# Performance work log

Measured on AMD Instinct MI355X. Metric: run time of the kernel, lower is better.

Reference implementation:

```python
import jax, jax.numpy as jnp
import numpy as np

QUALITY = 50

# standard JPEG luminance / chrominance quantization tables
_Y_TABLE = np.array([
    [16, 11, 10, 16, 24, 40, 51, 61],
    [12, 12, 14, 19, 26, 58, 60, 55],
    [14, 13, 16, 24, 40, 57, 69, 56],
    [14, 17, 22, 29, 51, 87, 80, 62],
    [18, 22, 37, 56, 68, 109, 103, 77],
    [24, 35, 55, 64, 81, 104, 113, 92],
    [49, 64, 78, 87, 103, 121, 120, 101],
    [72, 92, 95, 98, 112, 100, 103, 99]], dtype=np.float32)
_C_TABLE = np.full((8, 8), 99., dtype=np.float32)
_C_TABLE[:4, :4] = np.array([[17, 18, 24, 47], [18, 21, 26, 66],
                             [24, 26, 56, 99], [47, 66, 99, 99]], dtype=np.float32)

_i = np.arange(8)
_A = np.cos((2 * _i[:, None] + 1) * _i[None, :] * np.pi / 16).astype(np.float32)
_alpha = np.array([1.0 / np.sqrt(2)] + [1.0] * 7, dtype=np.float32)
_ALPHA2 = np.outer(_alpha, _alpha).astype(np.float32)        # idct pre-scale
_SCALE = (_ALPHA2 * 0.25).astype(np.float32)                 # dct post-scale

_RGB2YCC = np.array([[0.299, 0.587, 0.114],
                     [-0.168736, -0.331264, 0.5],
                     [0.5, -0.418688, -0.081312]], dtype=np.float32)
_SHIFT1 = np.array([0., 128., 128.], dtype=np.float32)
_YCC2RGB = np.array([[1., 0., 1.402],
                     [1., -0.344136, -0.714136],
                     [1., 1.772, 0.]], dtype=np.float32)
_SHIFT2 = np.array([0., -128., -128.], dtype=np.float32)


def _diff_round(x):
    r = jnp.round(x)
    return r + (x - r) ** 3


def _jpeg_channel(ch, table, factor):
    # ch: [B, h, w] -> blockwise DCT / quantize / dequant / IDCT -> [B, h, w]
    b, h, w = ch.shape
    blocks = ch.reshape(b, h // 8, 8, w // 8, 8).transpose(0, 1, 3, 2, 4).reshape(b, -1, 8, 8)
    A = jnp.asarray(_A)
    dct = jnp.asarray(_SCALE) * jnp.einsum('bnxy,xu,yv->bnuv', blocks - 128., A, A)
    qt = jnp.asarray(table) * factor
    q = _diff_round(dct / qt)
    deq = q * qt
    idct = 0.25 * jnp.einsum('bnuv,ux,vy->bnxy', deq * jnp.asarray(_ALPHA2), A, A) + 128.
    return idct.reshape(b, h // 8, w // 8, 8, 8).transpose(0, 1, 3, 2, 4).reshape(b, h, w)


def _diff_jpeg(x, quality):
    # quality -> scaling factor
    q = float(quality)
    factor = (5000. / q if q < 50 else 200. - 2. * q) / 100.
    x = jnp.clip(x, 0., 1.)
    img = jnp.transpose(x, (0, 2, 3, 1)) * 255.                      # [B,H,W,3]
    ycc = img @ jnp.asarray(_RGB2YCC).T + jnp.asarray(_SHIFT1)
    y, cb, cr = ycc[..., 0], ycc[..., 1], ycc[..., 2]
    b, h, w = y.shape
    # 4:2:0 chroma subsampling via 2x2 average pooling
    cb_s = cb.reshape(b, h // 2, 2, w // 2, 2).mean(axis=(2, 4))
    cr_s = cr.reshape(b, h // 2, 2, w // 2, 2).mean(axis=(2, 4))
    y2 = _jpeg_channel(y, _Y_TABLE, factor)
    cb2 = _jpeg_channel(cb_s, _C_TABLE, factor)
    cr2 = _jpeg_channel(cr_s, _C_TABLE, factor)
    cb_u = jnp.repeat(jnp.repeat(cb2, 2, axis=1), 2, axis=2)
    cr_u = jnp.repeat(jnp.repeat(cr2, 2, axis=1), 2, axis=2)
    ycc2 = jnp.stack([y2, cb_u, cr_u], axis=-1)
    rgb = (ycc2 + jnp.asarray(_SHIFT2)) @ jnp.asarray(_YCC2RGB).T
    rgb = jnp.clip(rgb, 0., 255.) / 255.
    out = jnp.transpose(rgb, (0, 3, 1, 2))                           # back to NCHW
    return jnp.clip(out, 0., 1.)


def setup_inputs() -> dict:
    key = jax.random.key(0)
    x = jax.random.uniform(key, (32, 3, 512, 512), dtype=jnp.float32)
    return {"x": x}


def reference(x):
    return _diff_jpeg(x, QUALITY)
```

## Files before the change

### kernel.cpp

```cpp
#include <hip/hip_runtime.h>
#include <math.h>

#define HH 512
#define WW 512

typedef float f2 __attribute__((ext_vector_type(2)));
typedef float f4 __attribute__((ext_vector_type(4)));

#define YS2  36
#define CS2  18
#define OY   0
#define OCB  576
#define OCR  720
#define OSCR 864
#define OAB  OSCR
#define WSZ  1272

static __device__ __forceinline__ f4 vclamp01x255(f4 v) {
    f4 z = 0.f, one = 1.f;
    return __builtin_elementwise_max(__builtin_elementwise_min(v, one), z) * 255.f;
}

__device__ __constant__ float YTAB[64] = {
    16,11,10,16,24,40,51,61,
    12,12,14,19,26,58,60,55,
    14,13,16,24,40,57,69,56,
    14,17,22,29,51,87,80,62,
    18,22,37,56,68,109,103,77,
    24,35,55,64,81,104,113,92,
    49,64,78,87,103,121,120,101,
    72,92,95,98,112,100,103,99};
__device__ __constant__ float CTAB[64] = {
    17,18,24,47,99,99,99,99,
    18,21,26,66,99,99,99,99,
    24,26,56,99,99,99,99,99,
    47,66,99,99,99,99,99,99,
    99,99,99,99,99,99,99,99,
    99,99,99,99,99,99,99,99,
    99,99,99,99,99,99,99,99,
    99,99,99,99,99,99,99,99};

__global__ __launch_bounds__(256) void jpeg_fused(const float* __restrict__ in,
                                                  float* __restrict__ out)
{
#pragma clang fp contract(off)
    __shared__ float Wall[4][WSZ];

    const int tid  = threadIdx.x;
    const int wid  = tid >> 6;
    const int lane = tid & 63;
    float* W = Wall[wid];

    const int wv    = blockIdx.x * 4 + wid;
    const int b     = wv >> 8;
    const int strip = (wv >> 3) & 31;
    const int seg   = wv & 7;
    const int h0    = strip * 16;
    const int w0    = seg * 64;
    const size_t plane = (size_t)HH * WW;

    const int rp  = lane >> 3;
    const int pr  = rp * 2;
    const int c4  = (lane & 7) * 4;
    const size_t grow   = ((size_t)b * 3 * HH + (size_t)(h0 + pr)) * WW + c4;
    const size_t gbase0 = grow + w0;
    const size_t gbase1 = grow + w0 + 32;

    const int g = lane >> 3, j = lane & 7;
    f2 As2[32];

    auto loadT = [&](f4* L, size_t gb) {
        L[0] = *(const f4*)(in + gb);
        L[1] = *(const f4*)(in + gb + WW);
        L[2] = *(const f4*)(in + gb + plane);
        L[3] = *(const f4*)(in + gb + plane + WW);
        L[4] = *(const f4*)(in + gb + 2 * plane);
        L[5] = *(const f4*)(in + gb + 2 * plane + WW);
    };

    auto stageT = [&](const f4* L) {
#pragma clang fp contract(off)
        f4 r0 = vclamp01x255(L[0]), r1 = vclamp01x255(L[1]);
        f4 g0 = vclamp01x255(L[2]), g1 = vclamp01x255(L[3]);
        f4 b0 = vclamp01x255(L[4]), b1 = vclamp01x255(L[5]);
        f4 y0  = ((r0 * 0.299f)     + (g0 * 0.587f))     + (b0 * 0.114f);
        f4 y1  = ((r1 * 0.299f)     + (g1 * 0.587f))     + (b1 * 0.114f);
        f4 cb0 = ((r0 * -0.168736f) + (g0 * -0.331264f)) + (b0 * 0.5f);
        f4 cb1 = ((r1 * -0.168736f) + (g1 * -0.331264f)) + (b1 * 0.5f);
        f4 cr0 = ((r0 * 0.5f)       + (g0 * -0.418688f)) + (b0 * -0.081312f);
        f4 cr1 = ((r1 * 0.5f)       + (g1 * -0.418688f)) + (b1 * -0.081312f);
        cb0 = cb0 + 128.f; cb1 = cb1 + 128.f;
        cr0 = cr0 + 128.f; cr1 = cr1 + 128.f;
        y0 = y0 - 128.f;  y1 = y1 - 128.f;
        *(f4*)&W[OY + pr * YS2 + c4]       = y0;
        *(f4*)&W[OY + (pr + 1) * YS2 + c4] = y1;
        f2 mb, mr;
        {
            float s01 = cb0.x + cb0.y, s23 = cb1.x + cb1.y;
            mb[0] = (s01 + s23) / 4.0f;
            float t01 = cb0.z + cb0.w, t23 = cb1.z + cb1.w;
            mb[1] = (t01 + t23) / 4.0f;
        }
        {
            float s01 = cr0.x + cr0.y, s23 = cr1.x + cr1.y;
            mr[0] = (s01 + s23) / 4.0f;
            float t01 = cr0.z + cr0.w, t23 = cr1.z + cr1.w;
            mr[1] = (t01 + t23) / 4.0f;
        }
        *(f2*)&W[OCB + rp * CS2 + (lane & 7) * 2] = mb;
        *(f2*)&W[OCR + rp * CS2 + (lane & 7) * 2] = mr;
    };

    auto dctAll = [&]() {
#pragma clang fp contract(off)
#pragma unroll
        for (int pass = 0; pass < 2; ++pass) {
            if (g < 6) {
                const int it   = pass * 6 + g;
                const bool isY = (it < 8);
                float* scr = &W[OSCR + g * 68];

                float X[8];
                int by = 0, bx = 0, ob = 0;
                if (isY) {
                    by = it >> 2; bx = it & 3;
#pragma unroll
                    for (int x = 0; x < 8; ++x)
                        X[x] = W[OY + (by * 8 + x) * YS2 + bx * 8 + j];
                } else {
                    ob = (it < 10) ? OCB : OCR;
                    bx = (it < 10) ? (it - 8) : (it - 10);
#pragma unroll
                    for (int x = 0; x < 8; ++x)
                        X[x] = W[ob + x * CS2 + bx * 8 + j] - 128.f;
                }

                f2 Tv[4];
#pragma unroll
                for (int m = 0; m < 4; ++m) {
                    f2 a = {0.f, 0.f};
#pragma unroll
                    for (int x = 0; x < 8; ++x) {
                        f2 xx = {X[x], X[x]};
                        a = __builtin_elementwise_fma(xx, As2[x * 4 + m], a);
                    }
                    Tv[m] = a;
                }
#pragma unroll
                for (int m = 0; m < 4; ++m) {
                    scr[(2 * m) * 8 + j]     = Tv[m][0];
                    scr[(2 * m + 1) * 8 + j] = Tv[m][1];
                }
                float Tt[8];
                {
                    float4 a = *(const float4*)&scr[j * 8];
                    float4 c = *(const float4*)&scr[j * 8 + 4];
                    Tt[0] = a.x; Tt[1] = a.y; Tt[2] = a.z; Tt[3] = a.w;
                    Tt[4] = c.x; Tt[5] = c.y; Tt[6] = c.z; Tt[7] = c.w;
                }
                float R[8];
#pragma unroll
                for (int m = 0; m < 4; ++m) {
                    f2 a = {0.f, 0.f};
#pragma unroll
                    for (int y = 0; y < 8; ++y) {
                        f2 tt = {Tt[y], Tt[y]};
                        a = __builtin_elementwise_fma(tt, As2[y * 4 + m], a);
                    }
                    R[2 * m] = a[0]; R[2 * m + 1] = a[1];
                }
                const float* QT = isY ? YTAB : CTAB;
                float qt[8];
                {
                    float4 a = *(const float4*)&QT[j * 8];
                    float4 c = *(const float4*)&QT[j * 8 + 4];
                    qt[0] = a.x; qt[1] = a.y; qt[2] = a.z; qt[3] = a.w;
                    qt[4] = c.x; qt[5] = c.y; qt[6] = c.z; qt[7] = c.w;
                }
                const float RC = 0.70710678118654752440f;
                float au = (j == 0) ? RC : 1.0f;
                float G[8];
#pragma unroll
                for (int v = 0; v < 8; ++v) {
                    float av    = (v == 0) ? RC : 1.0f;
                    float a2    = au * av;
                    float scale = a2 * 0.25f;
                    float dct   = scale * R[v];
                    float xq    = dct / qt[v];
                    float rd    = rintf(xq);
                    float d     = xq - rd;
                    float cube  = (d * d) * d;
                    float qq    = rd + cube;
                    float deq   = qq * qt[v];
                    G[v] = deq * a2;
                }
#pragma unroll
                for (int v = 0; v < 8; ++v) scr[v * 8 + j] = G[v];
                float Gt[8];
                {
                    float4 a = *(const float4*)&scr[j * 8];
                    float4 c = *(const float4*)&scr[j * 8 + 4];
                    Gt[0] = a.x; Gt[1] = a.y; Gt[2] = a.z; Gt[3] = a.w;
                    Gt[4] = c.x; Gt[5] = c.y; Gt[6] = c.z; Gt[7] = c.w;
                }
                f2 T2v[4];
#pragma unroll
                for (int m = 0; m < 4; ++m) {
                    f2 a = {0.f, 0.f};
#pragma unroll
                    for (int u = 0; u < 8; ++u) {
                        f2 gg = {Gt[u], Gt[u]};
                        a = __builtin_elementwise_fma(gg, As2[u * 4 + m], a);
                    }
                    T2v[m] = a;
                }
#pragma unroll
                for (int m = 0; m < 4; ++m) {
                    scr[(2 * m) * 8 + j]     = T2v[m][0];
                    scr[(2 * m + 1) * 8 + j] = T2v[m][1];
                }
                float T2t[8];
                {
                    float4 a = *(const float4*)&scr[j * 8];
                    float4 c = *(const float4*)&scr[j * 8 + 4];
                    T2t[0] = a.x; T2t[1] = a.y; T2t[2] = a.z; T2t[3] = a.w;
                    T2t[4] = c.x; T2t[5] = c.y; T2t[6] = c.z; T2t[7] = c.w;
                }
                float O[8];
#pragma unroll
                for (int m = 0; m < 4; ++m) {
                    f2 a = {0.f, 0.f};
#pragma unroll
                    for (int v = 0; v < 8; ++v) {
                        f2 tt = {T2t[v], T2t[v]};
                        a = __builtin_elementwise_fma(tt, As2[v * 4 + m], a);
                    }
                    a = (a * 0.25f) + 128.f;
                    O[2 * m] = a[0]; O[2 * m + 1] = a[1];
                }
                if (isY) {
                    *(f4*)&W[OY + (by * 8 + j) * YS2 + bx * 8]     = (f4){O[0], O[1], O[2], O[3]};
                    *(f4*)&W[OY + (by * 8 + j) * YS2 + bx * 8 + 4] = (f4){O[4], O[5], O[6], O[7]};
                } else {
                    *(f4*)&W[ob + j * CS2 + bx * 8]     = (f4){O[0], O[1], O[2], O[3]};
                    *(f4*)&W[ob + j * CS2 + bx * 8 + 4] = (f4){O[4], O[5], O[6], O[7]};
                }
            }
            asm volatile("" ::: "memory");
        }
    };

    auto outputT = [&](size_t gb) {
#pragma clang fp contract(off)
        const float INV255 = 1.0f / 255.0f;
        f4 ya = *(const f4*)&W[OY + pr * YS2 + c4];
        f4 yb = *(const f4*)&W[OY + (pr + 1) * YS2 + c4];
        f2 cbp = *(const f2*)&W[OCB + rp * CS2 + (lane & 7) * 2];
        f2 crp = *(const f2*)&W[OCR + rp * CS2 + (lane & 7) * 2];
        float cb0 = cbp[0] - 128.f, cb1 = cbp[1] - 128.f;
        float cr0 = crp[0] - 128.f, cr1 = crp[1] - 128.f;
        f4 cbm = {cb0, cb0, cb1, cb1};
        f4 crm = {cr0, cr0, cr1, cr1};
        f4 z = 0.f, m255 = 255.f;
#pragma unroll
        for (int row = 0; row < 2; ++row) {
            f4 yy = row ? yb : ya;
            f4 rv = yy + (crm * 1.402f);
            f4 gv = (yy + (cbm * -0.344136f)) + (crm * -0.714136f);
            f4 bv = yy + (cbm * 1.772f);
            rv = __builtin_elementwise_max(__builtin_elementwise_min(rv, m255), z) * INV255;
            gv = __builtin_elementwise_max(__builtin_elementwise_min(gv, m255), z) * INV255;
            bv = __builtin_elementwise_max(__builtin_elementwise_min(bv, m255), z) * INV255;
            size_t base = gb + (size_t)row * WW;
            __builtin_nontemporal_store(rv, (f4*)(out + base));
            __builtin_nontemporal_store(gv, (f4*)(out + base + plane));
            __builtin_nontemporal_store(bv, (f4*)(out + base + 2 * plane));
        }
    };

    f4 L1[6], L2[6];
    loadT(L1, gbase0);

    {
        int x = lane >> 3, u = lane & 7;
        double arg = (double)((2 * x + 1) * u) * 3.14159265358979323846 / 16.0;
        W[OAB + lane] = (float)cos(arg);
    }
#pragma unroll
    for (int k = 0; k < 32; ++k) {
        As2[k][0] = __int_as_float(__builtin_amdgcn_readfirstlane(__float_as_int(W[OAB + 2 * k])));
        As2[k][1] = __int_as_float(__builtin_amdgcn_readfirstlane(__float_as_int(W[OAB + 2 * k + 1])));
    }
    asm volatile("" ::: "memory");

    stageT(L1);
    loadT(L2, gbase1);
    asm volatile("" ::: "memory");
    dctAll();
    outputT(gbase0);
    asm volatile("" ::: "memory");
    stageT(L2);
    asm volatile("" ::: "memory");
    dctAll();
    outputT(gbase1);
}

extern "C" void kernel_launch(void* const* d_in, const int* in_sizes, int n_in,
                              void* d_out, int out_size, void* d_ws, size_t ws_size,
                              hipStream_t stream)
{
    const float* x = (const float*)d_in[0];
    float* o = (float*)d_out;
    int batch  = in_sizes[0] / (3 * HH * WW);
    int blocks = batch * 256 / 4;
    jpeg_fused<<<blocks, 256, 0, stream>>>(x, o);
}
```

Measured before the change: 41.00 us.

## Stage full 16x64 tile, run DCT in place across all lanes, use reciprocal quantization

Each wave now stages both 32-column halves into shared memory at once, with wider row strides, and issues both global loads up front. The blockwise DCT/IDCT then runs in three passes where all 8 lane-groups are busy: two Y passes and one chroma pass. Before, there were two passes of 6 active groups per half, four in all. The transposes reuse the block's own shared-memory region instead of a separate scratch area. Quantization division is replaced by a reciprocal multiply plus one Newton-style FMA correction, meant to match IEEE division, which cuts divide cost but raises shared-memory use per block (which may lower occupancy) and keeps more registers live for both loads.

```diff
diff --git a/kernel.cpp b/kernel.cpp
--- a/kernel.cpp
+++ b/kernel.cpp
@@ -7,14 +7,14 @@
 typedef float f2 __attribute__((ext_vector_type(2)));
 typedef float f4 __attribute__((ext_vector_type(4)));
 
-#define YS2  36
-#define CS2  18
+#define WFENCE() asm volatile("" ::: "memory")
+
+#define YS3  68
+#define CS3  36
 #define OY   0
-#define OCB  576
-#define OCR  720
-#define OSCR 864
-#define OAB  OSCR
-#define WSZ  1272
+#define OCB  1088
+#define OCR  1376
+#define WSZ  1664
 
 static __device__ __forceinline__ f4 vclamp01x255(f4 v) {
     f4 z = 0.f, one = 1.f;
@@ -39,6 +39,24 @@
     99,99,99,99,99,99,99,99,
     99,99,99,99,99,99,99,99,
     99,99,99,99,99,99,99,99};
+__device__ __constant__ float YINV[64] = {
+    1.f/16,1.f/11,1.f/10,1.f/16,1.f/24,1.f/40,1.f/51,1.f/61,
+    1.f/12,1.f/12,1.f/14,1.f/19,1.f/26,1.f/58,1.f/60,1.f/55,
+    1.f/14,1.f/13,1.f/16,1.f/24,1.f/40,1.f/57,1.f/69,1.f/56,
+    1.f/14,1.f/17,1.f/22,1.f/29,1.f/51,1.f/87,1.f/80,1.f/62,
+    1.f/18,1.f/22,1.f/37,1.f/56,1.f/68,1.f/109,1.f/103,1.f/77,
+    1.f/24,1.f/35,1.f/55,1.f/64,1.f/81,1.f/104,1.f/113,1.f/92,
+    1.f/49,1.f/64,1.f/78,1.f/87,1.f/103,1.f/121,1.f/120,1.f/101,
+    1.f/72,1.f/92,1.f/95,1.f/98,1.f/112,1.f/100,1.f/103,1.f/99};
+__device__ __constant__ float CINV[64] = {
+    1.f/17,1.f/18,1.f/24,1.f/47,1.f/99,1.f/99,1.f/99,1.f/99,
+    1.f/18,1.f/21,1.f/26,1.f/66,1.f/99,1.f/99,1.f/99,1.f/99,
+    1.f/24,1.f/26,1.f/56,1.f/99,1.f/99,1.f/99,1.f/99,1.f/99,
+    1.f/47,1.f/66,1.f/99,1.f/99,1.f/99,1.f/99,1.f/99,1.f/99,
+    1.f/99,1.f/99,1.f/99,1.f/99,1.f/99,1.f/99,1.f/99,1.f/99,
+    1.f/99,1.f/99,1.f/99,1.f/99,1.f/99,1.f/99,1.f/99,1.f/99,
+    1.f/99,1.f/99,1.f/99,1.f/99,1.f/99,1.f/99,1.f/99,1.f/99,
+    1.f/99,1.f/99,1.f/99,1.f/99,1.f/99,1.f/99,1.f/99,1.f/99};
 
 __global__ __launch_bounds__(256) void jpeg_fused(const float* __restrict__ in,
                                                   float* __restrict__ out)
@@ -61,7 +79,8 @@
 
     const int rp  = lane >> 3;
     const int pr  = rp * 2;
-    const int c4  = (lane & 7) * 4;
+    const int c8  = lane & 7;
+    const int c4  = c8 * 4;
     const size_t grow   = ((size_t)b * 3 * HH + (size_t)(h0 + pr)) * WW + c4;
     const size_t gbase0 = grow + w0;
     const size_t gbase1 = grow + w0 + 32;
@@ -78,7 +97,7 @@
         L[5] = *(const f4*)(in + gb + 2 * plane + WW);
     };
 
-    auto stageT = [&](const f4* L) {
+    auto stageT = [&](const f4* L, int P) {
 #pragma clang fp contract(off)
         f4 r0 = vclamp01x255(L[0]), r1 = vclamp01x255(L[1]);
         f4 g0 = vclamp01x255(L[2]), g1 = vclamp01x255(L[3]);
@@ -92,8 +111,8 @@
         cb0 = cb0 + 128.f; cb1 = cb1 + 128.f;
         cr0 = cr0 + 128.f; cr1 = cr1 + 128.f;
         y0 = y0 - 128.f;  y1 = y1 - 128.f;
-        *(f4*)&W[OY + pr * YS2 + c4]       = y0;
-        *(f4*)&W[OY + (pr + 1) * YS2 + c4] = y1;
+        *(f4*)&W[OY + pr * YS3 + 32 * P + c4]       = y0;
+        *(f4*)&W[OY + (pr + 1) * YS3 + 32 * P + c4] = y1;
         f2 mb, mr;
         {
             float s01 = cb0.x + cb0.y, s23 = cb1.x + cb1.y;
@@ -107,156 +126,147 @@
             float t01 = cr0.z + cr0.w, t23 = cr1.z + cr1.w;
             mr[1] = (t01 + t23) / 4.0f;
         }
-        *(f2*)&W[OCB + rp * CS2 + (lane & 7) * 2] = mb;
-        *(f2*)&W[OCR + rp * CS2 + (lane & 7) * 2] = mr;
+        *(f2*)&W[OCB + rp * CS3 + 16 * P + c8 * 2] = mb;
+        *(f2*)&W[OCR + rp * CS3 + 16 * P + c8 * 2] = mr;
     };
 
-    auto dctAll = [&]() {
+    auto dctBlock = [&](int Rb, int S, bool isY, bool isChroma) {
 #pragma clang fp contract(off)
-#pragma unroll
-        for (int pass = 0; pass < 2; ++pass) {
-            if (g < 6) {
-                const int it   = pass * 6 + g;
-                const bool isY = (it < 8);
-                float* scr = &W[OSCR + g * 68];
-
-                float X[8];
-                int by = 0, bx = 0, ob = 0;
-                if (isY) {
-                    by = it >> 2; bx = it & 3;
-#pragma unroll
-                    for (int x = 0; x < 8; ++x)
-                        X[x] = W[OY + (by * 8 + x) * YS2 + bx * 8 + j];
-                } else {
-                    ob = (it < 10) ? OCB : OCR;
-                    bx = (it < 10) ? (it - 8) : (it - 10);
-#pragma unroll
-                    for (int x = 0; x < 8; ++x)
-                        X[x] = W[ob + x * CS2 + bx * 8 + j] - 128.f;
-                }
-
-                f2 Tv[4];
-#pragma unroll
-                for (int m = 0; m < 4; ++m) {
-                    f2 a = {0.f, 0.f};
-#pragma unroll
-                    for (int x = 0; x < 8; ++x) {
-                        f2 xx = {X[x], X[x]};
-                        a = __builtin_elementwise_fma(xx, As2[x * 4 + m], a);
-                    }
-                    Tv[m] = a;
-                }
-#pragma unroll
-                for (int m = 0; m < 4; ++m) {
-                    scr[(2 * m) * 8 + j]     = Tv[m][0];
-                    scr[(2 * m + 1) * 8 + j] = Tv[m][1];
-                }
-                float Tt[8];
-                {
-                    float4 a = *(const float4*)&scr[j * 8];
-                    float4 c = *(const float4*)&scr[j * 8 + 4];
-                    Tt[0] = a.x; Tt[1] = a.y; Tt[2] = a.z; Tt[3] = a.w;
-                    Tt[4] = c.x; Tt[5] = c.y; Tt[6] = c.z; Tt[7] = c.w;
-                }
-                float R[8];
-#pragma unroll
-                for (int m = 0; m < 4; ++m) {
-                    f2 a = {0.f, 0.f};
-#pragma unroll
-                    for (int y = 0; y < 8; ++y) {
-                        f2 tt = {Tt[y], Tt[y]};
-                        a = __builtin_elementwise_fma(tt, As2[y * 4 + m], a);
-                    }
-                    R[2 * m] = a[0]; R[2 * m + 1] = a[1];
-                }
-                const float* QT = isY ? YTAB : CTAB;
-                float qt[8];
-                {
-                    float4 a = *(const float4*)&QT[j * 8];
-                    float4 c = *(const float4*)&QT[j * 8 + 4];
-                    qt[0] = a.x; qt[1] = a.y; qt[2] = a.z; qt[3] = a.w;
-                    qt[4] = c.x; qt[5] = c.y; qt[6] = c.z; qt[7] = c.w;
-                }
-                const float RC = 0.70710678118654752440f;
-                float au = (j == 0) ? RC : 1.0f;
-                float G[8];
-#pragma unroll
-                for (int v = 0; v < 8; ++v) {
-                    float av    = (v == 0) ? RC : 1.0f;
-                    float a2    = au * av;
-                    float scale = a2 * 0.25f;
-                    float dct   = scale * R[v];
-                    float xq    = dct / qt[v];
-                    float rd    = rintf(xq);
-                    float d     = xq - rd;
-                    float cube  = (d * d) * d;
-                    float qq    = rd + cube;
-                    float deq   = qq * qt[v];
-                    G[v] = deq * a2;
-                }
-#pragma unroll
-                for (int v = 0; v < 8; ++v) scr[v * 8 + j] = G[v];
-                float Gt[8];
-                {
-                    float4 a = *(const float4*)&scr[j * 8];
-                    float4 c = *(const float4*)&scr[j * 8 + 4];
-                    Gt[0] = a.x; Gt[1] = a.y; Gt[2] = a.z; Gt[3] = a.w;
-                    Gt[4] = c.x; Gt[5] = c.y; Gt[6] = c.z; Gt[7] = c.w;
-                }
-                f2 T2v[4];
-#pragma unroll
-                for (int m = 0; m < 4; ++m) {
-                    f2 a = {0.f, 0.f};
-#pragma unroll
-                    for (int u = 0; u < 8; ++u) {
-                        f2 gg = {Gt[u], Gt[u]};
-                        a = __builtin_elementwise_fma(gg, As2[u * 4 + m], a);
-                    }
-                    T2v[m] = a;
-                }
-#pragma unroll
-                for (int m = 0; m < 4; ++m) {
-                    scr[(2 * m) * 8 + j]     = T2v[m][0];
-                    scr[(2 * m + 1) * 8 + j] = T2v[m][1];
-                }
-                float T2t[8];
-                {
-                    float4 a = *(const float4*)&scr[j * 8];
-                    float4 c = *(const float4*)&scr[j * 8 + 4];
-                    T2t[0] = a.x; T2t[1] = a.y; T2t[2] = a.z; T2t[3] = a.w;
-                    T2t[4] = c.x; T2t[5] = c.y; T2t[6] = c.z; T2t[7] = c.w;
-                }
-                float O[8];
-#pragma unroll
-                for (int m = 0; m < 4; ++m) {
-                    f2 a = {0.f, 0.f};
-#pragma unroll
-                    for (int v = 0; v < 8; ++v) {
-                        f2 tt = {T2t[v], T2t[v]};
-                        a = __builtin_elementwise_fma(tt, As2[v * 4 + m], a);
-                    }
-                    a = (a * 0.25f) + 128.f;
-                    O[2 * m] = a[0]; O[2 * m + 1] = a[1];
-                }
-                if (isY) {
-                    *(f4*)&W[OY + (by * 8 + j) * YS2 + bx * 8]     = (f4){O[0], O[1], O[2], O[3]};
-                    *(f4*)&W[OY + (by * 8 + j) * YS2 + bx * 8 + 4] = (f4){O[4], O[5], O[6], O[7]};
-                } else {
-                    *(f4*)&W[ob + j * CS2 + bx * 8]     = (f4){O[0], O[1], O[2], O[3]};
-                    *(f4*)&W[ob + j * CS2 + bx * 8 + 4] = (f4){O[4], O[5], O[6], O[7]};
-                }
+        float X[8];
+#pragma unroll
+        for (int x = 0; x < 8; ++x) {
+            float v = W[Rb + x * S + j];
+            X[x] = isChroma ? (v - 128.f) : v;
+        }
+        WFENCE();
+        f2 Tv[4];
+#pragma unroll
+        for (int m = 0; m < 4; ++m) {
+            f2 a = {0.f, 0.f};
+#pragma unroll
+            for (int x = 0; x < 8; ++x) {
+                f2 xx = {X[x], X[x]};
+                a = __builtin_elementwise_fma(xx, As2[x * 4 + m], a);
             }
-            asm volatile("" ::: "memory");
-        }
+            Tv[m] = a;
+        }
+#pragma unroll
+        for (int m = 0; m < 4; ++m) {
+            W[Rb + (2 * m) * S + j]     = Tv[m][0];
+            W[Rb + (2 * m + 1) * S + j] = Tv[m][1];
+        }
+        WFENCE();
+        float Tt[8];
+        {
+            float4 a = *(const float4*)&W[Rb + j * S];
+            float4 c = *(const float4*)&W[Rb + j * S + 4];
+            Tt[0] = a.x; Tt[1] = a.y; Tt[2] = a.z; Tt[3] = a.w;
+            Tt[4] = c.x; Tt[5] = c.y; Tt[6] = c.z; Tt[7] = c.w;
+        }
+        WFENCE();
+        float R[8];
+#pragma unroll
+        for (int m = 0; m < 4; ++m) {
+            f2 a = {0.f, 0.f};
+#pragma unroll
+            for (int y = 0; y < 8; ++y) {
+                f2 tt = {Tt[y], Tt[y]};
+                a = __builtin_elementwise_fma(tt, As2[y * 4 + m], a);
+            }
+            R[2 * m] = a[0]; R[2 * m + 1] = a[1];
+        }
+        const float* QT = isY ? YTAB : CTAB;
+        const float* QI = isY ? YINV : CINV;
+        float qt[8], qi[8];
+        {
+            float4 a = *(const float4*)&QT[j * 8];
+            float4 c = *(const float4*)&QT[j * 8 + 4];
+            qt[0] = a.x; qt[1] = a.y; qt[2] = a.z; qt[3] = a.w;
+            qt[4] = c.x; qt[5] = c.y; qt[6] = c.z; qt[7] = c.w;
+            float4 ai = *(const float4*)&QI[j * 8];
+            float4 ci = *(const float4*)&QI[j * 8 + 4];
+            qi[0] = ai.x; qi[1] = ai.y; qi[2] = ai.z; qi[3] = ai.w;
+            qi[4] = ci.x; qi[5] = ci.y; qi[6] = ci.z; qi[7] = ci.w;
+        }
+        const float RC = 0.70710678118654752440f;
+        float au = (j == 0) ? RC : 1.0f;
+        float G[8];
+#pragma unroll
+        for (int v = 0; v < 8; ++v) {
+            float av    = (v == 0) ? RC : 1.0f;
+            float a2    = au * av;
+            float scale = a2 * 0.25f;
+            float dct   = scale * R[v];
+            float yv  = qi[v];
+            float q0  = dct * yv;
+            float rr  = fmaf(-qt[v], q0, dct);
+            float xq  = fmaf(rr, yv, q0);
+            float rd    = rintf(xq);
+            float d     = xq - rd;
+            float cube  = (d * d) * d;
+            float qq    = rd + cube;
+            float deq   = qq * qt[v];
+            G[v] = deq * a2;
+        }
+#pragma unroll
+        for (int v = 0; v < 8; ++v) W[Rb + v * S + j] = G[v];
+        WFENCE();
+        float Gt[8];
+        {
+            float4 a = *(const float4*)&W[Rb + j * S];
+            float4 c = *(const float4*)&W[Rb + j * S + 4];
+            Gt[0] = a.x; Gt[1] = a.y; Gt[2] = a.z; Gt[3] = a.w;
+            Gt[4] = c.x; Gt[5] = c.y; Gt[6] = c.z; Gt[7] = c.w;
+        }
+        WFENCE();
+        f2 T2v[4];
+#pragma unroll
+        for (int m = 0; m < 4; ++m) {
+            f2 a = {0.f, 0.f};
+#pragma unroll
+            for (int u = 0; u < 8; ++u) {
+                f2 gg = {Gt[u], Gt[u]};
+                a = __builtin_elementwise_fma(gg, As2[u * 4 + m], a);
+            }
+            T2v[m] = a;
+        }
+#pragma unroll
+        for (int m = 0; m < 4; ++m) {
+            W[Rb + (2 * m) * S + j]     = T2v[m][0];
+            W[Rb + (2 * m + 1) * S + j] = T2v[m][1];
+        }
+        WFENCE();
+        float T2t[8];
+        {
+            float4 a = *(const float4*)&W[Rb + j * S];
+            float4 c = *(const float4*)&W[Rb + j * S + 4];
+            T2t[0] = a.x; T2t[1] = a.y; T2t[2] = a.z; T2t[3] = a.w;
+            T2t[4] = c.x; T2t[5] = c.y; T2t[6] = c.z; T2t[7] = c.w;
+        }
+        WFENCE();
+        float O[8];
+#pragma unroll
+        for (int m = 0; m < 4; ++m) {
+            f2 a = {0.f, 0.f};
+#pragma unroll
+            for (int v = 0; v < 8; ++v) {
+                f2 tt = {T2t[v], T2t[v]};
+                a = __builtin_elementwise_fma(tt, As2[v * 4 + m], a);
+            }
+            a = (a * 0.25f) + 128.f;
+            O[2 * m] = a[0]; O[2 * m + 1] = a[1];
+        }
+        *(f4*)&W[Rb + j * S]     = (f4){O[0], O[1], O[2], O[3]};
+        *(f4*)&W[Rb + j * S + 4] = (f4){O[4], O[5], O[6], O[7]};
     };
 
-    auto outputT = [&](size_t gb) {
+    auto outputT = [&](size_t gb, int P) {
 #pragma clang fp contract(off)
         const float INV255 = 1.0f / 255.0f;
-        f4 ya = *(const f4*)&W[OY + pr * YS2 + c4];
-        f4 yb = *(const f4*)&W[OY + (pr + 1) * YS2 + c4];
-        f2 cbp = *(const f2*)&W[OCB + rp * CS2 + (lane & 7) * 2];
-        f2 crp = *(const f2*)&W[OCR + rp * CS2 + (lane & 7) * 2];
+        f4 ya = *(const f4*)&W[OY + pr * YS3 + 32 * P + c4];
+        f4 yb = *(const f4*)&W[OY + (pr + 1) * YS3 + 32 * P + c4];
+        f2 cbp = *(const f2*)&W[OCB + rp * CS3 + 16 * P + c8 * 2];
+        f2 crp = *(const f2*)&W[OCR + rp * CS3 + 16 * P + c8 * 2];
         float cb0 = cbp[0] - 128.f, cb1 = cbp[1] - 128.f;
         float cr0 = crp[0] - 128.f, cr1 = crp[1] - 128.f;
         f4 cbm = {cb0, cb0, cb1, cb1};
@@ -280,29 +290,37 @@
 
     f4 L1[6], L2[6];
     loadT(L1, gbase0);
+    loadT(L2, gbase1);
 
     {
         int x = lane >> 3, u = lane & 7;
         double arg = (double)((2 * x + 1) * u) * 3.14159265358979323846 / 16.0;
-        W[OAB + lane] = (float)cos(arg);
+        W[OCB + lane] = (float)cos(arg);
     }
+    WFENCE();
 #pragma unroll
     for (int k = 0; k < 32; ++k) {
-        As2[k][0] = __int_as_float(__builtin_amdgcn_readfirstlane(__float_as_int(W[OAB + 2 * k])));
-        As2[k][1] = __int_as_float(__builtin_amdgcn_readfirstlane(__float_as_int(W[OAB + 2 * k + 1])));
+        As2[k][0] = __int_as_float(__builtin_amdgcn_readfirstlane(__float_as_int(W[OCB + 2 * k])));
+        As2[k][1] = __int_as_float(__builtin_amdgcn_readfirstlane(__float_as_int(W[OCB + 2 * k + 1])));
     }
-    asm volatile("" ::: "memory");
-
-    stageT(L1);
-    loadT(L2, gbase1);
-    asm volatile("" ::: "memory");
-    dctAll();
-    outputT(gbase0);
-    asm volatile("" ::: "memory");
-    stageT(L2);
-    asm volatile("" ::: "memory");
-    dctAll();
-    outputT(gbase1);
+    WFENCE();
+
+    stageT(L1, 0);
+    stageT(L2, 1);
+    WFENCE();
+
+    dctBlock(OY + 0 * 544 + 8 * g, YS3, true, false);
+    WFENCE();
+    dctBlock(OY + 1 * 544 + 8 * g, YS3, true, false);
+    WFENCE();
+    {
+        int Rb = (g < 4) ? (OCB + 8 * g) : (OCR + 8 * (g - 4));
+        dctBlock(Rb, CS3, false, true);
+    }
+    WFENCE();
+
+    outputT(gbase0, 0);
+    outputT(gbase1, 1);
 }
 
 extern "C" void kernel_launch(void* const* d_in, const int* in_sizes, int n_in,
```

Result: faster. 36.37 us (-11.3%).
